# Optimization experiments

Hardware: AMD Instinct MI355X
Metric: run time of the kernel (lower is better)

Reference implementation:

```python
import jax, jax.numpy as jnp
import numpy as np

EPS = 1e-5

def layer_norm(x, w, b):
    mu = jnp.mean(x, axis=-1, keepdims=True)
    var = jnp.var(x, axis=-1, keepdims=True)
    return (x - mu) / jnp.sqrt(var + EPS) * w + b

def setup_inputs() -> dict:
    key = jax.random.key(0)
    B, N, C = 4, 4096, 1024
    H = 16
    MW = 4 * C
    ks = jax.random.split(key, 8)
    s = 0.02
    return {
        "x": jax.random.normal(ks[0], (B, N, C), dtype=jnp.float32),
        "ln1_w": jnp.ones((C,), jnp.float32), "ln1_b": jnp.zeros((C,), jnp.float32),
        "q_w": jax.random.normal(ks[1], (C, C), jnp.float32) * s, "q_b": jnp.zeros((C,), jnp.float32),
        "k_w": jax.random.normal(ks[2], (C, C), jnp.float32) * s, "k_b": jnp.zeros((C,), jnp.float32),
        "v_w": jax.random.normal(ks[3], (C, C), jnp.float32) * s, "v_b": jnp.zeros((C,), jnp.float32),
        "o_w": jax.random.normal(ks[4], (C, C), jnp.float32) * s, "o_b": jnp.zeros((C,), jnp.float32),
        "ln2_w": jnp.ones((C,), jnp.float32), "ln2_b": jnp.zeros((C,), jnp.float32),
        "fc_w": jax.random.normal(ks[5], (MW, C), jnp.float32) * s, "fc_b": jnp.zeros((MW,), jnp.float32),
        "proj_w": jax.random.normal(ks[6], (C, MW), jnp.float32) * s, "proj_b": jnp.zeros((C,), jnp.float32),
    }

def reference(x, ln1_w, ln1_b, q_w, q_b, k_w, k_b, v_w, v_b, o_w, o_b,
              ln2_w, ln2_b, fc_w, fc_b, proj_w, proj_b):
    B, N, C = x.shape
    H = 16
    D = C // H
    xn = layer_norm(x, ln1_w, ln1_b)
    # projections, reshape to (B, N, H, D), transpose to (B, H, N, D)
    q = (xn @ q_w.T + q_b).reshape(B, N, H, D).transpose(0, 2, 1, 3)
    k = (xn @ k_w.T + k_b).reshape(B, N, H, D).transpose(0, 2, 1, 3)
    v = (xn @ v_w.T + v_b).reshape(B, N, H, D).transpose(0, 2, 1, 3)
    # faithful to original: einsum labels treat the HEAD axis as contraction axis
    q = jax.nn.elu(q) + 1.0
    k = jax.nn.elu(k) + 1.0
    kv = jnp.einsum('bhnd,bhne->bnde', k, v)            # sum over heads -> (B,N,D,D)
    qkv = jnp.einsum('bhnd,bnde->bhne', q, kv)          # (B,H,N,D)
    k_sum = k.sum(axis=1)                               # sum over heads -> (B,N,D)
    qk = jnp.einsum('bhnd,bnd->bhn', q, k_sum)          # (B,H,N)
    attn = qkv / qk[..., None]                          # (B,H,N,D)
    attn = attn.transpose(0, 2, 1, 3).reshape(B, N, C)
    attn = attn @ o_w.T + o_b
    x = x + attn
    xn2 = layer_norm(x, ln2_w, ln2_b)
    h = jax.nn.gelu(xn2 @ fc_w.T + fc_b, approximate=False)
    x = x + (h @ proj_w.T + proj_b)
    return x
```

## Files before the change

### kernel.cpp

```cpp
#include <hip/hip_runtime.h>
#include <math.h>

typedef unsigned short u16;
typedef unsigned int   u32;
typedef __attribute__((ext_vector_type(8))) short bf16x8;
typedef __attribute__((ext_vector_type(4))) float f32x4;
typedef __attribute__((ext_vector_type(4))) unsigned short u16x4;

__device__ __forceinline__ float bf2f(u16 v){ return __uint_as_float(((u32)v) << 16); }
__device__ __forceinline__ u16 f2bf(float f){
  u32 u = __float_as_uint(f);
  return (u16)((u + 0x7fffu + ((u >> 16) & 1u)) >> 16);
}
__device__ __forceinline__ float elu1(float x){ return x > 0.f ? x + 1.f : __expf(x); }
__device__ __forceinline__ float gelu_f(float v){
  float u = 0.7978845608f * (v + 0.044715f * v * v * v);
  float e = __expf(-2.f * fabsf(u));
  float th = copysignf((1.f - e) / (1.f + e), u);
  return 0.5f * v * (1.f + th);
}

__global__ __launch_bounds__(256) void k_cast(const float* __restrict__ src, u16* __restrict__ dst, int n4){
  int i = blockIdx.x * 256 + threadIdx.x;
  int stride = gridDim.x * 256;
  for (; i < n4; i += stride){
    float4 v = ((const float4*)src)[i];
    u16x4 o; o.x = f2bf(v.x); o.y = f2bf(v.y); o.z = f2bf(v.z); o.w = f2bf(v.w);
    ((u16x4*)dst)[i] = o;
  }
}

__global__ void k_cat3(const float* __restrict__ a, const float* __restrict__ b,
                       const float* __restrict__ c, float* __restrict__ dst){
  int i = blockIdx.x * 256 + threadIdx.x;
  dst[i] = i < 1024 ? a[i] : (i < 2048 ? b[i - 1024] : c[i - 2048]);
}

__global__ __launch_bounds__(256) void k_ln(const float* __restrict__ x, const float* __restrict__ w,
                                            const float* __restrict__ b, u16* __restrict__ out){
  const int t = threadIdx.x;
  const size_t m = blockIdx.x;
  float4 v = ((const float4*)(x + m * 1024))[t];
  float s  = v.x + v.y + v.z + v.w;
  float s2 = v.x*v.x + v.y*v.y + v.z*v.z + v.w*v.w;
  #pragma unroll
  for (int o = 32; o > 0; o >>= 1){ s += __shfl_down(s, o, 64); s2 += __shfl_down(s2, o, 64); }
  __shared__ float red[8];
  if ((t & 63) == 0){ red[t >> 6] = s; red[4 + (t >> 6)] = s2; }
  __syncthreads();
  s  = red[0] + red[1] + red[2] + red[3];
  s2 = red[4] + red[5] + red[6] + red[7];
  float mu  = s * (1.f / 1024.f);
  float inv = rsqrtf(s2 * (1.f / 1024.f) - mu * mu + 1e-5f);
  float4 wv = ((const float4*)w)[t];
  float4 bv = ((const float4*)b)[t];
  u16x4 o;
  o.x = f2bf((v.x - mu) * inv * wv.x + bv.x);
  o.y = f2bf((v.y - mu) * inv * wv.y + bv.y);
  o.z = f2bf((v.z - mu) * inv * wv.z + bv.z);
  o.w = f2bf((v.w - mu) * inv * wv.w + bv.w);
  ((u16x4*)(out + m * 1024))[t] = o;
}

__global__ __launch_bounds__(256) void k_attn(const u16* __restrict__ qkv, u16* __restrict__ out){
  __shared__ float qe[4][16][68];
  __shared__ float ke[4][16][68];
  __shared__ float sm[4][16][20];
  const int w = threadIdx.x >> 6, lane = threadIdx.x & 63;
  const size_t m = (size_t)blockIdx.x * 4 + w;
  const u16* base = qkv + m * 3072;
  #pragma unroll
  for (int i = 0; i < 8; ++i){
    int idx = i * 64 + lane;
    int h = idx >> 5, c2 = (idx & 31) * 2;
    u32 qv = ((const u32*)base)[idx];
    u32 kv = ((const u32*)base)[512 + idx];
    float2 qf, kf;
    qf.x = elu1(bf2f((u16)(qv & 0xffffu))); qf.y = elu1(bf2f((u16)(qv >> 16)));
    kf.x = elu1(bf2f((u16)(kv & 0xffffu))); kf.y = elu1(bf2f((u16)(kv >> 16)));
    *(float2*)&qe[w][h][c2] = qf;
    *(float2*)&ke[w][h][c2] = kf;
  }
  float vr[16];
  #pragma unroll
  for (int h = 0; h < 16; ++h) vr[h] = bf2f(base[2048 + h * 64 + lane]);
  __syncthreads();
  const int sh = lane >> 2, jb = lane & 3;
  float sacc[4] = {0.f, 0.f, 0.f, 0.f};
  #pragma unroll
  for (int d4 = 0; d4 < 16; ++d4){
    float4 q4 = *(const float4*)&qe[w][sh][d4 * 4];
    #pragma unroll
    for (int j = 0; j < 4; ++j){
      float4 k4 = *(const float4*)&ke[w][4 * jb + j][d4 * 4];
      sacc[j] += q4.x*k4.x + q4.y*k4.y + q4.z*k4.z + q4.w*k4.w;
    }
  }
  #pragma unroll
  for (int j = 0; j < 4; ++j) sm[w][sh][4 * jb + j] = sacc[j];
  float part = sacc[0] + sacc[1] + sacc[2] + sacc[3];
  part += __shfl_xor(part, 1, 64);
  part += __shfl_xor(part, 2, 64);
  if (jb == 0) sm[w][sh][16] = part;
  __syncthreads();
  float acc[16];
  #pragma unroll
  for (int h = 0; h < 16; ++h) acc[h] = 0.f;
  #pragma unroll
  for (int h = 0; h < 16; ++h){
    #pragma unroll
    for (int j4 = 0; j4 < 4; ++j4){
      float4 s4 = *(const float4*)&sm[w][h][j4 * 4];
      acc[h] += s4.x*vr[4*j4] + s4.y*vr[4*j4+1] + s4.z*vr[4*j4+2] + s4.w*vr[4*j4+3];
    }
  }
  u16* ob = out + m * 1024;
  #pragma unroll
  for (int h = 0; h < 16; ++h)
    ob[h * 64 + lane] = f2bf(acc[h] / sm[w][h][16]);
}

template<int QM, int QN>
__device__ __forceinline__ void quad16(f32x4 (&acc)[8][4], const bf16x8 (&a)[4][2], const bf16x8 (&b)[2][2]){
  __builtin_amdgcn_s_setprio(1);
  #pragma unroll
  for (int s = 0; s < 2; ++s)
    #pragma unroll
    for (int i = 0; i < 4; ++i)
      #pragma unroll
      for (int j = 0; j < 2; ++j)
        acc[QM*4+i][QN*2+j] = __builtin_amdgcn_mfma_f32_16x16x32_bf16(a[i][s], b[j][s], acc[QM*4+i][QN*2+j], 0, 0, 0);
  __builtin_amdgcn_s_setprio(0);
}

template<int EPI>
__global__ __launch_bounds__(512, 2) void k_gemm(const u16* __restrict__ A, const u16* __restrict__ W,
                                                 const float* __restrict__ bias, const float* __restrict__ res,
                                                 void* __restrict__ outp, int N, int K, int nbn){
  __shared__ alignas(16) char lds[131072];
  const int tid  = threadIdx.x;
  const int lane = tid & 63, wid = tid >> 6;
  const int wr = wid >> 2, wc = wid & 3;
  const int g = lane >> 4, l15 = lane & 15;
  const int nwg = gridDim.x, bid = blockIdx.x;
  const int swz = (bid & 7) * (nwg >> 3) + (bid >> 3);
  const int m0 = (swz / nbn) * 256, n0 = (swz % nbn) * 256;
  const u16* gA = A + (size_t)m0 * K;
  const u16* gW = W + (size_t)n0 * K;
  const int nt = K >> 6;

  f32x4 acc[8][4];
  #pragma unroll
  for (int i = 0; i < 8; ++i)
    #pragma unroll
    for (int j = 0; j < 4; ++j) acc[i][j] = (f32x4){0.f, 0.f, 0.f, 0.f};

  auto stageA = [&](int b, int kt, int h){
    char* dst = lds + b * 65536 + h * 16384 + wid * 1024;
    const u16* src = gA + (size_t)(h * 128) * K + (kt << 6);
    #pragma unroll
    for (int i = 0; i < 2; ++i){
      int li = i * 512 + tid;
      int r  = li >> 3;
      int ch = (li & 7) ^ (r & 7);
      __builtin_amdgcn_global_load_lds(
        (const __attribute__((address_space(1))) u32*)(src + (size_t)r * K + ch * 8),
        (__attribute__((address_space(3))) u32*)(dst + i * 8192), 16, 0, 0);
    }
  };
  auto stageB = [&](int b, int kt, int h){
    char* dst = lds + b * 65536 + 32768 + h * 16384 + wid * 1024;
    const u16* src = gW + (size_t)(h * 128) * K + (kt << 6);
    #pragma unroll
    for (int i = 0; i < 2; ++i){
      int li = i * 512 + tid;
      int r  = li >> 3;
      int ch = (li & 7) ^ (r & 7);
      __builtin_amdgcn_global_load_lds(
        (const __attribute__((address_space(1))) u32*)(src + (size_t)r * K + ch * 8),
        (__attribute__((address_space(3))) u32*)(dst + i * 8192), 16, 0, 0);
    }
  };
  auto rdA4 = [&](bf16x8 (&d)[4][2], const char* Abase, int qm){
    #pragma unroll
    for (int i = 0; i < 4; ++i)
      #pragma unroll
      for (int s = 0; s < 2; ++s){
        int row = wr * 128 + (qm * 4 + i) * 16 + l15;
        d[i][s] = *(const bf16x8*)(Abase + row * 128 + (((4 * s + g) ^ (row & 7)) << 4));
      }
  };
  auto rdB2 = [&](bf16x8 (&d)[2][2], const char* Bbase, int qn){
    #pragma unroll
    for (int j = 0; j < 2; ++j)
      #pragma unroll
      for (int s = 0; s < 2; ++s){
        int row = wc * 64 + (qn * 2 + j) * 16 + l15;
        d[j][s] = *(const bf16x8*)(Bbase + row * 128 + (((4 * s + g) ^ (row & 7)) << 4));
      }
  };

  bf16x8 aA[4][2];
  bf16x8 bB[2][2][2];

  stageA(0, 0, 0); stageA(0, 0, 1); stageB(0, 0, 0); stageB(0, 0, 1);
  if (nt > 1){
    stageA(1, 1, 0); stageA(1, 1, 1);
    asm volatile("s_waitcnt vmcnt(4)" ::: "memory");
  } else {
    asm volatile("s_waitcnt vmcnt(0)" ::: "memory");
  }
  __builtin_amdgcn_s_barrier();

  for (int t = 0; t < nt; ++t){
    const int c = t & 1;
    const char* Ab = lds + c * 65536;
    const char* Bb = Ab + 32768;

    rdB2(bB[0], Bb, 0);
    rdA4(aA, Ab, 0);
    if (t + 1 < nt) stageB(c ^ 1, t + 1, 0);
    __builtin_amdgcn_s_barrier();
    asm volatile("s_waitcnt lgkmcnt(0)" ::: "memory");
    quad16<0, 0>(acc, aA, bB[0]);
    __builtin_amdgcn_s_barrier();

    rdB2(bB[1], Bb, 1);
    if (t + 1 < nt) stageB(c ^ 1, t + 1, 1);
    __builtin_amdgcn_s_barrier();
    asm volatile("s_waitcnt lgkmcnt(0)" ::: "memory");
    quad16<0, 1>(acc, aA, bB[1]);
    __builtin_amdgcn_s_barrier();

    rdA4(aA, Ab, 1);
    __builtin_amdgcn_s_barrier();
    asm volatile("s_waitcnt lgkmcnt(0)" ::: "memory");
    quad16<1, 0>(acc, aA, bB[0]);
    __builtin_amdgcn_s_barrier();

    if (t + 2 < nt){ stageA(c, t + 2, 0); stageA(c, t + 2, 1); }
    __builtin_amdgcn_s_barrier();
    quad16<1, 1>(acc, aA, bB[1]);
    if (t + 2 < nt){
      asm volatile("s_waitcnt vmcnt(4)" ::: "memory");
    } else {
      asm volatile("s_waitcnt vmcnt(0)" ::: "memory");
    }
    __builtin_amdgcn_s_barrier();
  }

  #pragma unroll
  for (int mf = 0; mf < 8; ++mf){
    #pragma unroll
    for (int nf = 0; nf < 4; ++nf){
      int row = m0 + wr * 128 + mf * 16 + 4 * g;
      int col = n0 + wc * 64 + nf * 16 + l15;
      float bcol = bias[col];
      #pragma unroll
      for (int r = 0; r < 4; ++r){
        float v = acc[mf][nf][r] + bcol;
        size_t idx = (size_t)(row + r) * N + col;
        if constexpr (EPI == 0){
          ((u16*)outp)[idx] = f2bf(v);
        } else if constexpr (EPI == 1){
          ((float*)outp)[idx] = res[idx] + v;
        } else if constexpr (EPI == 2){
          ((u16*)outp)[idx] = f2bf(gelu_f(v));
        } else {
          float* o = (float*)outp; o[idx] = o[idx] + v;
        }
      }
    }
  }
}

extern "C" void kernel_launch(void* const* d_in, const int* in_sizes, int n_in,
                              void* d_out, int out_size, void* d_ws, size_t ws_size,
                              hipStream_t stream){
  (void)in_sizes; (void)n_in; (void)out_size; (void)ws_size;
  const float* x    = (const float*)d_in[0];
  const float* ln1w = (const float*)d_in[1];
  const float* ln1b = (const float*)d_in[2];
  const float* qw   = (const float*)d_in[3];
  const float* qb   = (const float*)d_in[4];
  const float* kw   = (const float*)d_in[5];
  const float* kb   = (const float*)d_in[6];
  const float* vw   = (const float*)d_in[7];
  const float* vb   = (const float*)d_in[8];
  const float* ow   = (const float*)d_in[9];
  const float* ob   = (const float*)d_in[10];
  const float* ln2w = (const float*)d_in[11];
  const float* ln2b = (const float*)d_in[12];
  const float* fcw  = (const float*)d_in[13];
  const float* fcb  = (const float*)d_in[14];
  const float* pw   = (const float*)d_in[15];
  const float* pb   = (const float*)d_in[16];

  char* ws = (char*)d_ws;
  u16*   WQKV = (u16*)(ws + 0);
  u16*   WO   = (u16*)(ws + 6291456);
  u16*   WFC  = (u16*)(ws + 8388608);
  u16*   WPR  = (u16*)(ws + 16777216);
  float* BQ   = (float*)(ws + 25165824);
  u16*   XN   = (u16*)(ws + 25178112);
  u16*   QKV  = (u16*)(ws + 58732544);
  u16*   ATT  = (u16*)(ws + 159395840);
  u16*   H    = QKV;
  float* OUT  = (float*)d_out;

  k_cast<<<512, 256, 0, stream>>>(qw, WQKV,           262144);
  k_cast<<<512, 256, 0, stream>>>(kw, WQKV + 1048576, 262144);
  k_cast<<<512, 256, 0, stream>>>(vw, WQKV + 2097152, 262144);
  k_cast<<<512, 256, 0, stream>>>(ow, WO,             262144);
  k_cast<<<1024, 256, 0, stream>>>(fcw, WFC,          1048576);
  k_cast<<<1024, 256, 0, stream>>>(pw,  WPR,          1048576);
  k_cat3<<<12, 256, 0, stream>>>(qb, kb, vb, BQ);

  k_ln<<<16384, 256, 0, stream>>>(x, ln1w, ln1b, XN);
  k_gemm<0><<<64 * 12, 512, 0, stream>>>(XN, WQKV, BQ, nullptr, QKV, 3072, 1024, 12);
  k_attn<<<4096, 256, 0, stream>>>(QKV, ATT);
  k_gemm<1><<<64 * 4, 512, 0, stream>>>(ATT, WO, ob, x, OUT, 1024, 1024, 4);

  k_ln<<<16384, 256, 0, stream>>>(OUT, ln2w, ln2b, XN);
  k_gemm<2><<<64 * 16, 512, 0, stream>>>(XN, WFC, fcb, nullptr, H, 4096, 1024, 16);
  k_gemm<3><<<64 * 4, 512, 0, stream>>>(H, WPR, pb, nullptr, OUT, 1024, 4096, 4);
}
```

Before: 580.6 us.

## Split GEMM MFMA phases along K and software-pipeline LDS fragment reads

Reorganizes the GEMM main loop so each MFMA phase covers one K-half (s) across all four N fragments instead of one N-half across both K-halves. LDS fragment reads for the next phase, and the first phase of the next tile, are issued before the current MFMAs, with partial lgkmcnt waits instead of full drains. This is meant to hide LDS read latency behind MFMA work and drops one barrier per iteration. It relies on correct lgkmcnt accounting and on the ordering around stageA overwriting buffer c, and it uses extra registers for the double-buffered fragments.

```diff
diff --git a/kernel.cpp b/kernel.cpp
--- a/kernel.cpp
+++ b/kernel.cpp
@@ -120,16 +120,14 @@
     ob[h * 64 + lane] = f2bf(acc[h] / sm[w][h][16]);
 }
 
-template<int QM, int QN>
-__device__ __forceinline__ void quad16(f32x4 (&acc)[8][4], const bf16x8 (&a)[4][2], const bf16x8 (&b)[2][2]){
+template<int QM>
+__device__ __forceinline__ void quad16(f32x4 (&acc)[8][4], const bf16x8 (&a)[4], const bf16x8 (&b)[4]){
   __builtin_amdgcn_s_setprio(1);
   #pragma unroll
-  for (int s = 0; s < 2; ++s)
-    #pragma unroll
-    for (int i = 0; i < 4; ++i)
-      #pragma unroll
-      for (int j = 0; j < 2; ++j)
-        acc[QM*4+i][QN*2+j] = __builtin_amdgcn_mfma_f32_16x16x32_bf16(a[i][s], b[j][s], acc[QM*4+i][QN*2+j], 0, 0, 0);
+  for (int i = 0; i < 4; ++i)
+    #pragma unroll
+    for (int nf = 0; nf < 4; ++nf)
+      acc[QM*4+i][nf] = __builtin_amdgcn_mfma_f32_16x16x32_bf16(a[i], b[nf], acc[QM*4+i][nf], 0, 0, 0);
   __builtin_amdgcn_s_setprio(0);
 }
 
@@ -181,27 +179,23 @@
         (__attribute__((address_space(3))) u32*)(dst + i * 8192), 16, 0, 0);
     }
   };
-  auto rdA4 = [&](bf16x8 (&d)[4][2], const char* Abase, int qm){
-    #pragma unroll
-    for (int i = 0; i < 4; ++i)
-      #pragma unroll
-      for (int s = 0; s < 2; ++s){
-        int row = wr * 128 + (qm * 4 + i) * 16 + l15;
-        d[i][s] = *(const bf16x8*)(Abase + row * 128 + (((4 * s + g) ^ (row & 7)) << 4));
-      }
+  auto rdA = [&](bf16x8 (&d)[4], const char* Abase, int qm, int s){
+    #pragma unroll
+    for (int i = 0; i < 4; ++i){
+      int row = wr * 128 + (qm * 4 + i) * 16 + l15;
+      d[i] = *(const bf16x8*)(Abase + row * 128 + (((4 * s + g) ^ (row & 7)) << 4));
+    }
   };
-  auto rdB2 = [&](bf16x8 (&d)[2][2], const char* Bbase, int qn){
-    #pragma unroll
-    for (int j = 0; j < 2; ++j)
-      #pragma unroll
-      for (int s = 0; s < 2; ++s){
-        int row = wc * 64 + (qn * 2 + j) * 16 + l15;
-        d[j][s] = *(const bf16x8*)(Bbase + row * 128 + (((4 * s + g) ^ (row & 7)) << 4));
-      }
+  auto rdB = [&](bf16x8 (&d)[4], const char* Bbase, int s){
+    #pragma unroll
+    for (int nf = 0; nf < 4; ++nf){
+      int row = wc * 64 + nf * 16 + l15;
+      d[nf] = *(const bf16x8*)(Bbase + row * 128 + (((4 * s + g) ^ (row & 7)) << 4));
+    }
   };
 
-  bf16x8 aA[4][2];
-  bf16x8 bB[2][2][2];
+  bf16x8 aP0[4], aP1[4];
+  bf16x8 bS0[4], bS1[4];
 
   stageA(0, 0, 0); stageA(0, 0, 1); stageB(0, 0, 0); stageB(0, 0, 1);
   if (nt > 1){
@@ -211,42 +205,50 @@
     asm volatile("s_waitcnt vmcnt(0)" ::: "memory");
   }
   __builtin_amdgcn_s_barrier();
+  rdA(aP0, lds, 0, 0);
+  rdB(bS0, lds + 32768, 0);
 
   for (int t = 0; t < nt; ++t){
     const int c = t & 1;
     const char* Ab = lds + c * 65536;
     const char* Bb = Ab + 32768;
-
-    rdB2(bB[0], Bb, 0);
-    rdA4(aA, Ab, 0);
+    const char* AbN = lds + (c ^ 1) * 65536;
+    const char* BbN = AbN + 32768;
+
+    rdA(aP1, Ab, 0, 1);
+    rdB(bS1, Bb, 1);
     if (t + 1 < nt) stageB(c ^ 1, t + 1, 0);
     __builtin_amdgcn_s_barrier();
+    asm volatile("s_waitcnt lgkmcnt(8)" ::: "memory");
+    quad16<0>(acc, aP0, bS0);
+    __builtin_amdgcn_s_barrier();
+
+    rdA(aP0, Ab, 1, 0);
+    if (t + 1 < nt) stageB(c ^ 1, t + 1, 1);
+    __builtin_amdgcn_s_barrier();
+    asm volatile("s_waitcnt lgkmcnt(4)" ::: "memory");
+    quad16<0>(acc, aP1, bS1);
+    __builtin_amdgcn_s_barrier();
+
+    rdA(aP1, Ab, 1, 1);
+    __builtin_amdgcn_s_barrier();
+    asm volatile("s_waitcnt lgkmcnt(4)" ::: "memory");
+    quad16<1>(acc, aP0, bS0);
     asm volatile("s_waitcnt lgkmcnt(0)" ::: "memory");
-    quad16<0, 0>(acc, aA, bB[0]);
-    __builtin_amdgcn_s_barrier();
-
-    rdB2(bB[1], Bb, 1);
-    if (t + 1 < nt) stageB(c ^ 1, t + 1, 1);
-    __builtin_amdgcn_s_barrier();
-    asm volatile("s_waitcnt lgkmcnt(0)" ::: "memory");
-    quad16<0, 1>(acc, aA, bB[1]);
-    __builtin_amdgcn_s_barrier();
-
-    rdA4(aA, Ab, 1);
-    __builtin_amdgcn_s_barrier();
-    asm volatile("s_waitcnt lgkmcnt(0)" ::: "memory");
-    quad16<1, 0>(acc, aA, bB[0]);
     __builtin_amdgcn_s_barrier();
 
     if (t + 2 < nt){ stageA(c, t + 2, 0); stageA(c, t + 2, 1); }
-    __builtin_amdgcn_s_barrier();
-    quad16<1, 1>(acc, aA, bB[1]);
+    quad16<1>(acc, aP1, bS1);
     if (t + 2 < nt){
       asm volatile("s_waitcnt vmcnt(4)" ::: "memory");
     } else {
       asm volatile("s_waitcnt vmcnt(0)" ::: "memory");
     }
     __builtin_amdgcn_s_barrier();
+    if (t + 1 < nt){
+      rdA(aP0, AbN, 0, 0);
+      rdB(bS0, BbN, 0);
+    }
   }
 
   #pragma unroll
```

After: 571.4 us. Within noise of the previous version (-1.6%).
